# Optimization experiments

Hardware: AMD Instinct MI355X
Metric: run time of the kernel (lower is better)

## Reference

```python
import jax, jax.numpy as jnp
import numpy as np

EPS = 1e-06
BANDWIDTH = 0.1  # scipy minimize x0; frozen on first forward in the original


def _pairwise_sqdist(a, b):
    # a: [B, N, 3], b: [B, M, 3] -> [B, N, M] squared euclidean distances
    a2 = jnp.sum(a * a, axis=-1)  # [B, N]
    b2 = jnp.sum(b * b, axis=-1)  # [B, M]
    ab = jnp.einsum('bnd,bmd->bnm', a, b)  # [B, N, M]
    return jnp.maximum(a2[:, :, None] + b2[:, None, :] - 2.0 * ab, 0.0)


def _compute_density(points, bandwidth):
    # Gaussian KDE over all pairs (self included), normalized by N-1,
    # matching compute_density in the torch source.
    n = points.shape[1]
    sqd = _pairwise_sqdist(points, points)  # [B, N, N]
    kde = jnp.exp(-0.5 * sqd / (bandwidth * bandwidth))
    return jnp.sum(kde, axis=2) / (n - 1)  # [B, N]


def setup_inputs() -> dict:
    key = jax.random.key(0)
    k1, k2 = jax.random.split(key)
    predicted = jax.random.normal(k1, (8, 4096, 3), dtype=jnp.float32)
    ground_truth = jax.random.normal(k2, (8, 4096, 3), dtype=jnp.float32)
    return {
        'predicted': predicted,
        'ground_truth': ground_truth,
        'bandwidth_pred': jnp.float32(BANDWIDTH),
        'bandwidth_gt': jnp.float32(BANDWIDTH),
    }


def reference(predicted, ground_truth, bandwidth_pred, bandwidth_gt):
    # Chamfer distance: per-point squared distance to nearest neighbor in the
    # other cloud (standard ChamferDistance CUDA ext returns squared dists).
    sqd = _pairwise_sqdist(predicted, ground_truth)  # [B, N, M]
    dist_pred_to_gt = jnp.min(sqd, axis=2)  # [B, N]
    dist_gt_to_pred = jnp.min(sqd, axis=1)  # [B, M]

    density_pred = _compute_density(predicted, bandwidth_pred)  # [B, N]
    density_gt = _compute_density(ground_truth, bandwidth_gt)   # [B, M]

    loss_pred_to_gt = jnp.mean(dist_pred_to_gt / (density_pred + EPS))
    loss_gt_to_pred = jnp.mean(dist_gt_to_pred / (density_gt + EPS))
    return loss_pred_to_gt + loss_gt_to_pred
```

## Files before the change

### kernel.cpp

```cpp
#include <hip/hip_runtime.h>


#define NPTS 4096
#define NB   8
#define TS   128
#define TPB  256
#define NT   32
#define BIGF 3.4e38f

#define DCHUNKS    144
#define DENS_BLKS  (16*DCHUNKS)
#define CROSS_BLKS 2048
#define PTSTOT (NB*NPTS)
#define TRIVEC 496

__device__ __forceinline__ void unpack8(const float4* s4, int base,
                                        float (&X)[8], float (&Y)[8], float (&Z)[8])
{
    float4 A = s4[base+0], B = s4[base+1], C = s4[base+2];
    float4 D = s4[base+3], E = s4[base+4], F = s4[base+5];
    X[0]=A.x; Y[0]=A.y; Z[0]=A.z;  X[1]=A.w; Y[1]=B.x; Z[1]=B.y;
    X[2]=B.z; Y[2]=B.w; Z[2]=C.x;  X[3]=C.y; Y[3]=C.z; Z[3]=C.w;
    X[4]=D.x; Y[4]=D.y; Z[4]=D.z;  X[5]=D.w; Y[5]=E.x; Z[5]=E.y;
    X[6]=E.z; Y[6]=E.w; Z[6]=F.x;  X[7]=F.y; Y[7]=F.z; Z[7]=F.w;
}

__global__ __launch_bounds__(TPB) void dacl_pairs(
    const float* __restrict__ pred, const float* __restrict__ gt,
    const float* __restrict__ bwp,  const float* __restrict__ bwg,
    float* __restrict__ minP2Gp,
    float* __restrict__ minG2Pp,
    float* __restrict__ densCol,
    float* __restrict__ densRow)
{
    __shared__ float4 sCol[384];
    __shared__ float4 sRow[96];
    __shared__ float  sRed[384];

    const int tid  = threadIdx.x;
    const int ty   = tid & 15;
    const int tx   = tid >> 4;
    const int wave = tid >> 6;
    const int lane = tid & 63;
    const int bid  = blockIdx.x;

    if (bid < DENS_BLKS) {
        const int cb = bid / DCHUNKS;
        int rem      = bid - cb * DCHUNKS;
        const int b  = cb & 7;
        const int cl = cb >> 3;

        int u = 0;
        int nc = 8;
        while (rem >= nc) { rem -= nc; ++u; nc = (35 - u) >> 2; }
        const int cj = rem;
        const int js = cj * 4;
        const int steps = 32 - u;
        const int je = (js + 4 < steps) ? js + 4 : steps;
        const int nT = je - js;

        const float* __restrict__ P = cl ? gt : pred;
        float* __restrict__ dCol = densCol + (size_t)(cl*NB + b) * (TRIVEC*TS);
        float* __restrict__ dRow = densRow + (size_t)(cj*2 + cl) * PTSTOT + b*NPTS;
        const float bw = cl ? bwg[0] : bwp[0];
        const float sc = sqrtf(0.5f / (bw*bw*0.6931471805599453f));

        const float4* cb4 = (const float4*)(P + (size_t)b*NPTS*3);

        if (tid < 96) {
            float4 v = cb4[u*96 + tid];
            v.x*=sc; v.y*=sc; v.z*=sc; v.w*=sc;  sRow[tid] = v;
        }
        for (int i = tid; i < nT*96; i += TPB) {
            float4 v = cb4[(u + js)*96 + i];
            v.x*=sc; v.y*=sc; v.z*=sc; v.w*=sc;  sCol[i] = v;
        }
        __syncthreads();

        float rx[8], ry[8], rz[8], nrr[8], racc[8];
        unpack8(sRow, ty*6, rx, ry, rz);
        #pragma unroll
        for (int r = 0; r < 8; ++r) {
            nrr[r]  = -fmaf(rx[r],rx[r], fmaf(ry[r],ry[r], rz[r]*rz[r]));
            racc[r] = 0.0f;
        }

        for (int j = js; j < je; ++j) {
            const int t  = j - js;
            const int TV = u + j;

            float cx[8], cy[8], cz[8];
            unpack8(sCol, t*96 + tx*6, cx, cy, cz);

            if (j == 0) {
                #pragma unroll
                for (int c = 0; c < 8; ++c) {
                    const float ax = 2.0f*cx[c], ay = 2.0f*cy[c], az = 2.0f*cz[c];
                    const float ncc = fmaf(-cx[c],cx[c],
                                      fmaf(-cy[c],cy[c], -cz[c]*cz[c]));
                    #pragma unroll
                    for (int r = 0; r < 8; ++r) {
                        float e = fmaf(ax, rx[r], ncc);
                        e = fmaf(ay, ry[r], e);
                        e = fmaf(az, rz[r], e);
                        racc[r] += __builtin_amdgcn_exp2f(e + nrr[r]);
                    }
                }
            } else {
                float cacc[8];
                #pragma unroll
                for (int c = 0; c < 8; ++c) cacc[c] = 0.0f;
                #pragma unroll
                for (int c = 0; c < 8; ++c) {
                    const float ax = 2.0f*cx[c], ay = 2.0f*cy[c], az = 2.0f*cz[c];
                    const float ncc = fmaf(-cx[c],cx[c],
                                      fmaf(-cy[c],cy[c], -cz[c]*cz[c]));
                    #pragma unroll
                    for (int r = 0; r < 8; ++r) {
                        float e = fmaf(ax, rx[r], ncc);
                        e = fmaf(ay, ry[r], e);
                        e = fmaf(az, rz[r], e);
                        const float k = __builtin_amdgcn_exp2f(e + nrr[r]);
                        racc[r] += k;
                        cacc[c] += k;
                    }
                }
                const int triTV = (TV*(TV-1)) >> 1;
                #pragma unroll
                for (int c = 0; c < 8; ++c) {
                    float v = cacc[c];
                    v += __shfl_xor(v, 1, 64);
                    v += __shfl_xor(v, 2, 64);
                    v += __shfl_xor(v, 4, 64);
                    v += __shfl_xor(v, 8, 64);
                    if (ty == 0)
                        dCol[(triTV + u)*TS + tx*8 + c] = v;
                }
            }
        }
        {
            float vv[8];
            #pragma unroll
            for (int r = 0; r < 8; ++r) {
                float v = racc[r];
                v += __shfl_xor(v, 16, 64);
                v += __shfl_xor(v, 32, 64);
                vv[r] = v;
            }
            __syncthreads();
            if (wave > 0 && lane < 16) {
                #pragma unroll
                for (int r = 0; r < 8; ++r)
                    sRed[(wave-1)*128 + lane*8 + r] = vv[r];
            }
            __syncthreads();
            if (wave == 0 && lane < 16) {
                #pragma unroll
                for (int r = 0; r < 8; ++r) {
                    const int o = lane*8 + r;
                    dRow[u*TS + o] = (vv[r] + sRed[o])
                                   + (sRed[128+o] + sRed[256+o]);
                }
            }
        }
    } else {
        const int cb = bid - DENS_BLKS;
        const int b  = cb >> 8;
        const int I  = (cb >> 3) & 31;
        const int ph = cb & 7;

        const float4* pb4 = (const float4*)(pred + (size_t)b*NPTS*3);
        const float4* gb4 = (const float4*)(gt   + (size_t)b*NPTS*3);
        if (tid < 96) sRow[tid] = pb4[I*96 + tid];
        #pragma unroll
        for (int i = 0; i < 2; ++i) {
            const int o = tid + i*TPB;
            if (o < 384) sCol[o] = gb4[ph*384 + o];
        }
        __syncthreads();

        float rx[8], ry[8], rz[8], rr[8], rmin[8];
        unpack8(sRow, ty*6, rx, ry, rz);
        #pragma unroll
        for (int r = 0; r < 8; ++r) {
            rr[r]   = fmaf(rx[r],rx[r], fmaf(ry[r],ry[r], rz[r]*rz[r]));
            rmin[r] = BIGF;
        }
        float* __restrict__ mg = minG2Pp + (size_t)I*PTSTOT + b*NPTS;

        for (int t = 0; t < 4; ++t) {
            float cx[8], cy[8], cz[8], cmin[8];
            unpack8(sCol, t*96 + tx*6, cx, cy, cz);
            #pragma unroll
            for (int c = 0; c < 8; ++c) cmin[c] = BIGF;
            #pragma unroll
            for (int c2 = 0; c2 < 4; ++c2) {
                const int c0 = 2*c2, c1 = c0 + 1;
                const float ax0 = -2.0f*cx[c0], ay0 = -2.0f*cy[c0], az0 = -2.0f*cz[c0];
                const float cc0 = fmaf(cx[c0],cx[c0], fmaf(cy[c0],cy[c0], cz[c0]*cz[c0]));
                const float ax1 = -2.0f*cx[c1], ay1 = -2.0f*cy[c1], az1 = -2.0f*cz[c1];
                const float cc1 = fmaf(cx[c1],cx[c1], fmaf(cy[c1],cy[c1], cz[c1]*cz[c1]));
                #pragma unroll
                for (int r2 = 0; r2 < 4; ++r2) {
                    const int r0 = 2*r2, r1 = r0 + 1;
                    float t00 = fmaf(ax0, rx[r0], cc0);
                    t00 = fmaf(ay0, ry[r0], t00); t00 = fmaf(az0, rz[r0], t00);
                    float t01 = fmaf(ax1, rx[r0], cc1);
                    t01 = fmaf(ay1, ry[r0], t01); t01 = fmaf(az1, rz[r0], t01);
                    float t10 = fmaf(ax0, rx[r1], cc0);
                    t10 = fmaf(ay0, ry[r1], t10); t10 = fmaf(az0, rz[r1], t10);
                    float t11 = fmaf(ax1, rx[r1], cc1);
                    t11 = fmaf(ay1, ry[r1], t11); t11 = fmaf(az1, rz[r1], t11);
                    rmin[r0] = fminf(rmin[r0], fminf(t00, t01));
                    rmin[r1] = fminf(rmin[r1], fminf(t10, t11));
                    const float d00 = t00 + rr[r0], d01 = t01 + rr[r0];
                    const float d10 = t10 + rr[r1], d11 = t11 + rr[r1];
                    cmin[c0] = fminf(cmin[c0], fminf(d00, d10));
                    cmin[c1] = fminf(cmin[c1], fminf(d01, d11));
                }
            }
            #pragma unroll
            for (int c = 0; c < 8; ++c) {
                float v = cmin[c];
                v = fminf(v, __shfl_xor(v, 1, 64));
                v = fminf(v, __shfl_xor(v, 2, 64));
                v = fminf(v, __shfl_xor(v, 4, 64));
                v = fminf(v, __shfl_xor(v, 8, 64));
                if (ty == 0)
                    mg[(ph*4+t)*TS + tx*8 + c] = v;
            }
        }
        float vv[8];
        #pragma unroll
        for (int r = 0; r < 8; ++r) {
            float v = rmin[r] + rr[r];
            v = fminf(v, __shfl_xor(v, 16, 64));
            v = fminf(v, __shfl_xor(v, 32, 64));
            vv[r] = v;
        }
        __syncthreads();
        if (wave > 0 && lane < 16) {
            #pragma unroll
            for (int r = 0; r < 8; ++r) sRed[(wave-1)*128 + lane*8 + r] = vv[r];
        }
        __syncthreads();
        if (wave == 0 && lane < 16) {
            #pragma unroll
            for (int r = 0; r < 8; ++r) {
                const int o = lane*8 + r;
                minP2Gp[(size_t)ph*PTSTOT + b*NPTS + I*TS + o] =
                    fminf(fminf(vv[r], sRed[o]),
                          fminf(sRed[128+o], sRed[256+o]));
            }
        }
    }
}

__global__ __launch_bounds__(256) void dacl_combine(
    const float* __restrict__ minP2Gp, const float* __restrict__ minG2Pp,
    const float* __restrict__ densCol, const float* __restrict__ densRow,
    float* __restrict__ bsum)
{
    const int g   = blockIdx.x * 256 + threadIdx.x;
    const int dir = g >> 15;
    const int idx = g & 32767;
    const int b   = idx >> 12;
    const int pt  = idx & 4095;
    const int T   = pt >> 7;
    const int co  = pt & 127;
    const int cl  = dir;

    float m = BIGF;
    if (dir == 0) {
        #pragma unroll
        for (int s = 0; s < 8; ++s) m = fminf(m, minP2Gp[(size_t)s*PTSTOT + idx]);
    } else {
        #pragma unroll
        for (int s = 0; s < 32; ++s) m = fminf(m, minG2Pp[(size_t)s*PTSTOT + idx]);
    }
    m = fmaxf(m, 0.0f);

    float dn = 0.0f;
    const float* dC = densCol + (size_t)(cl*NB + b)*(TRIVEC*TS)
                      + ((T*(T-1)) >> 1)*TS + co;
    for (int RT = 0; RT < T; ++RT) dn += dC[RT*TS];
    const int ncj = (35 - T) >> 2;
    #pragma unroll
    for (int cj = 0; cj < 8; ++cj) {
        if (cj < ncj) dn += densRow[(size_t)(cj*2 + cl)*PTSTOT + idx];
    }

    float val = m / (dn * (1.0f/4095.0f) + 1e-6f) * (1.0f/32768.0f);

    #pragma unroll
    for (int off = 32; off; off >>= 1) val += __shfl_down(val, off);
    __shared__ float sm[4];
    const int lane = threadIdx.x & 63, wid = threadIdx.x >> 6;
    if (lane == 0) sm[wid] = val;
    __syncthreads();
    if (threadIdx.x == 0) bsum[blockIdx.x] = (sm[0] + sm[1]) + (sm[2] + sm[3]);
}

__global__ __launch_bounds__(256) void dacl_final(
    const float* __restrict__ bsum, float* __restrict__ out)
{
    float v = bsum[threadIdx.x];
    #pragma unroll
    for (int off = 32; off; off >>= 1) v += __shfl_down(v, off);
    __shared__ float sm[4];
    const int lane = threadIdx.x & 63, wid = threadIdx.x >> 6;
    if (lane == 0) sm[wid] = v;
    __syncthreads();
    if (threadIdx.x == 0) out[0] = (sm[0] + sm[1]) + (sm[2] + sm[3]);
}

extern "C" void kernel_launch(void* const* d_in, const int* in_sizes, int n_in,
                              void* d_out, int out_size, void* d_ws, size_t ws_size,
                              hipStream_t stream)
{
    const float* pred = (const float*)d_in[0];
    const float* gt   = (const float*)d_in[1];
    const float* bwp  = (const float*)d_in[2];
    const float* bwg  = (const float*)d_in[3];

    float* minP2Gp = (float*)d_ws;
    float* minG2Pp = minP2Gp + (size_t)8*PTSTOT;
    float* densCol = minG2Pp + (size_t)32*PTSTOT;
    float* densRow = densCol + (size_t)16*TRIVEC*TS;
    float* bsum    = densRow + (size_t)16*PTSTOT;

    dacl_pairs<<<DENS_BLKS + CROSS_BLKS, TPB, 0, stream>>>(
        pred, gt, bwp, bwg, minP2Gp, minG2Pp, densCol, densRow);
    dacl_combine<<<256, 256, 0, stream>>>(minP2Gp, minG2Pp, densCol, densRow, bsum);
    dacl_final<<<1, 256, 0, stream>>>(bsum, (float*)d_out);
}
```

Baseline: 88.86 us.

## Morton-sort point clouds and cull tile pairs using AABB bounds

Adds a pre-pass that bins each cloud into a 16^3 grid, sorts the points by Morton code and records a bounding box for every 128-point tile. A second pre-pass computes per-tile upper bounds on nearest-neighbour distance. The density loop skips tile pairs whose Gaussian terms would all fall below about 2^-30. The chamfer loop skips tile pairs whose box gap exceeds both tiles' upper bounds, so it cannot contain a nearest neighbour. The goal is to remove most of the quadratic pair work, at the cost of three extra kernel launches, a buffer-initialization pass and a small truncation error in the density sums.

```diff
diff --git a/kernel.cpp b/kernel.cpp
--- a/kernel.cpp
+++ b/kernel.cpp
@@ -5,8 +5,9 @@
 #define NB   8
 #define TS   128
 #define TPB  256
-#define NT   32
 #define BIGF 3.4e38f
+#define LN2f 0.6931471805599453f
+#define SKIP_THR 30.0f
 
 #define DCHUNKS    144
 #define DENS_BLKS  (16*DCHUNKS)
@@ -25,9 +26,144 @@
     X[6]=E.z; Y[6]=E.w; Z[6]=F.x;  X[7]=F.y; Y[7]=F.z; Z[7]=F.w;
 }
 
+__device__ __forceinline__ float aabbGap2(const float* A, const float* B)
+{
+    float g, s;
+    g = fmaxf(0.f, fmaxf(B[0]-A[4], A[0]-B[4])); s = g*g;
+    g = fmaxf(0.f, fmaxf(B[1]-A[5], A[1]-B[5])); s = fmaf(g,g,s);
+    g = fmaxf(0.f, fmaxf(B[2]-A[6], A[2]-B[6])); s = fmaf(g,g,s);
+    return s;
+}
+
+__global__ __launch_bounds__(1024) void dacl_sort(
+    const float* __restrict__ pred, const float* __restrict__ gt,
+    float* __restrict__ sortedP,
+    float* __restrict__ aabb)
+{
+    __shared__ int h[4096];
+    __shared__ int wsum[16];
+    const int tid  = threadIdx.x;
+    const int lane = tid & 63, wid = tid >> 6;
+    const int cb   = blockIdx.x;
+    const int b    = cb & 7, cl = cb >> 3;
+    const float* src = (cl ? gt : pred) + (size_t)b*NPTS*3;
+    float* dst = sortedP + (size_t)cb*NPTS*3;
+
+    for (int i = tid; i < 4096; i += 1024) h[i] = 0;
+    __syncthreads();
+
+    float px[4], py[4], pz[4]; int code[4];
+    #pragma unroll
+    for (int k = 0; k < 4; ++k) {
+        const int i = k*1024 + tid;
+        const float x = src[i*3], y = src[i*3+1], z = src[i*3+2];
+        px[k]=x; py[k]=y; pz[k]=z;
+        int cx = (int)floorf((x + 4.8f) * (1.0f/0.6f));
+        int cy = (int)floorf((y + 4.8f) * (1.0f/0.6f));
+        int cz = (int)floorf((z + 4.8f) * (1.0f/0.6f));
+        cx = min(max(cx,0),15); cy = min(max(cy,0),15); cz = min(max(cz,0),15);
+        int m = 0;
+        #pragma unroll
+        for (int bit = 0; bit < 4; ++bit)
+            m |= (((cx>>bit)&1)<<(3*bit)) | (((cy>>bit)&1)<<(3*bit+1))
+               | (((cz>>bit)&1)<<(3*bit+2));
+        code[k] = m;
+        atomicAdd(&h[m], 1);
+    }
+    __syncthreads();
+
+    const int a0=h[4*tid], a1=h[4*tid+1], a2=h[4*tid+2], a3=h[4*tid+3];
+    const int tot = a0+a1+a2+a3;
+    int v = tot;
+    #pragma unroll
+    for (int off = 1; off < 64; off <<= 1) {
+        int n = __shfl_up(v, off, 64);
+        if (lane >= off) v += n;
+    }
+    if (lane == 63) wsum[wid] = v;
+    __syncthreads();
+    if (tid == 0) {
+        int run = 0;
+        for (int i = 0; i < 16; ++i) { int t = wsum[i]; wsum[i] = run; run += t; }
+    }
+    __syncthreads();
+    const int excl = wsum[wid] + v - tot;
+    h[4*tid]   = excl;
+    h[4*tid+1] = excl + a0;
+    h[4*tid+2] = excl + a0 + a1;
+    h[4*tid+3] = excl + a0 + a1 + a2;
+    __syncthreads();
+
+    #pragma unroll
+    for (int k = 0; k < 4; ++k) {
+        const int pos = atomicAdd(&h[code[k]], 1);
+        dst[pos*3]   = px[k];
+        dst[pos*3+1] = py[k];
+        dst[pos*3+2] = pz[k];
+    }
+    __threadfence();
+    __syncthreads();
+
+    {
+        const int t = tid >> 5, j = tid & 31;
+        float mnx=BIGF,mny=BIGF,mnz=BIGF,mxx=-BIGF,mxy=-BIGF,mxz=-BIGF;
+        #pragma unroll
+        for (int kk = 0; kk < 4; ++kk) {
+            const int i = t*128 + j*4 + kk;
+            const float x = dst[i*3], y = dst[i*3+1], z = dst[i*3+2];
+            mnx=fminf(mnx,x); mny=fminf(mny,y); mnz=fminf(mnz,z);
+            mxx=fmaxf(mxx,x); mxy=fmaxf(mxy,y); mxz=fmaxf(mxz,z);
+        }
+        #pragma unroll
+        for (int off = 1; off < 32; off <<= 1) {
+            mnx=fminf(mnx,__shfl_xor(mnx,off,64));
+            mny=fminf(mny,__shfl_xor(mny,off,64));
+            mnz=fminf(mnz,__shfl_xor(mnz,off,64));
+            mxx=fmaxf(mxx,__shfl_xor(mxx,off,64));
+            mxy=fmaxf(mxy,__shfl_xor(mxy,off,64));
+            mxz=fmaxf(mxz,__shfl_xor(mxz,off,64));
+        }
+        if (j == 0) {
+            float* o = aabb + (size_t)(cb*32 + t)*8;
+            o[0]=mnx; o[1]=mny; o[2]=mnz; o[3]=0.f;
+            o[4]=mxx; o[5]=mxy; o[6]=mxz; o[7]=0.f;
+        }
+    }
+}
+
+__global__ __launch_bounds__(256) void dacl_prep2(
+    const float* __restrict__ sortedP, float* __restrict__ UB)
+{
+    const int g = blockIdx.x*256 + threadIdx.x;
+    const int b = g >> 12, i = g & 4095;
+    const float* ps = sortedP + (size_t)b*12288;
+    const float* gs = sortedP + (size_t)(8+b)*12288;
+    const float dx = ps[i*3]-gs[i*3], dy = ps[i*3+1]-gs[i*3+1],
+                dz = ps[i*3+2]-gs[i*3+2];
+    float d2 = dx*dx + dy*dy + dz*dz;
+    const int lane = threadIdx.x & 63, wid = threadIdx.x >> 6;
+    #pragma unroll
+    for (int off = 1; off < 64; off <<= 1)
+        d2 = fmaxf(d2, __shfl_xor(d2, off, 64));
+    __shared__ float wmax[4];
+    if (lane == 0) wmax[wid] = d2;
+    __syncthreads();
+    if (threadIdx.x == 0)   UB[blockIdx.x*2]     = fmaxf(wmax[0], wmax[1]);
+    if (threadIdx.x == 128) UB[blockIdx.x*2 + 1] = fmaxf(wmax[2], wmax[3]);
+}
+
+__global__ __launch_bounds__(256) void dacl_init(
+    float* __restrict__ minG2Pp, float* __restrict__ densCol)
+{
+    const int g = blockIdx.x*256 + threadIdx.x;
+    minG2Pp[g] = BIGF;
+    if (g < 16*TRIVEC*TS) densCol[g] = 0.0f;
+}
+
 __global__ __launch_bounds__(TPB) void dacl_pairs(
-    const float* __restrict__ pred, const float* __restrict__ gt,
-    const float* __restrict__ bwp,  const float* __restrict__ bwg,
+    const float* __restrict__ sortedP, const float* __restrict__ aabb,
+    const float* __restrict__ UB,
+    const float* __restrict__ bwp, const float* __restrict__ bwg,
     float* __restrict__ minP2Gp,
     float* __restrict__ minG2Pp,
     float* __restrict__ densCol,
@@ -50,8 +186,7 @@
         const int b  = cb & 7;
         const int cl = cb >> 3;
 
-        int u = 0;
-        int nc = 8;
+        int u = 0, nc = 8;
         while (rem >= nc) { rem -= nc; ++u; nc = (35 - u) >> 2; }
         const int cj = rem;
         const int js = cj * 4;
@@ -59,13 +194,15 @@
         const int je = (js + 4 < steps) ? js + 4 : steps;
         const int nT = je - js;
 
-        const float* __restrict__ P = cl ? gt : pred;
-        float* __restrict__ dCol = densCol + (size_t)(cl*NB + b) * (TRIVEC*TS);
+        const float* __restrict__ P = sortedP + (size_t)cb*12288;
+        float* __restrict__ dCol = densCol + (size_t)cb * (TRIVEC*TS);
         float* __restrict__ dRow = densRow + (size_t)(cj*2 + cl) * PTSTOT + b*NPTS;
         const float bw = cl ? bwg[0] : bwp[0];
-        const float sc = sqrtf(0.5f / (bw*bw*0.6931471805599453f));
-
-        const float4* cb4 = (const float4*)(P + (size_t)b*NPTS*3);
+        const float s2raw = 0.5f / (bw*bw*LN2f);
+        const float sc = sqrtf(s2raw);
+        const float* myAB = aabb + (size_t)(cb*32 + u)*8;
+
+        const float4* cb4 = (const float4*)P;
 
         if (tid < 96) {
             float4 v = cb4[u*96 + tid];
@@ -88,6 +225,11 @@
         for (int j = js; j < je; ++j) {
             const int t  = j - js;
             const int TV = u + j;
+
+            if (j > 0) {
+                const float* cAB = aabb + (size_t)(cb*32 + TV)*8;
+                if (s2raw * aabbGap2(myAB, cAB) > SKIP_THR) continue;
+            }
 
             float cx[8], cy[8], cz[8];
             unpack8(sCol, t*96 + tx*6, cx, cy, cz);
@@ -169,8 +311,11 @@
         const int I  = (cb >> 3) & 31;
         const int ph = cb & 7;
 
-        const float4* pb4 = (const float4*)(pred + (size_t)b*NPTS*3);
-        const float4* gb4 = (const float4*)(gt   + (size_t)b*NPTS*3);
+        const float4* pb4 = (const float4*)(sortedP + (size_t)b*12288);
+        const float4* gb4 = (const float4*)(sortedP + (size_t)(8+b)*12288);
+        const float* pAB  = aabb + (size_t)(b*32 + I)*8;
+        const float  UB_I = UB[b*32 + I];
+
         if (tid < 96) sRow[tid] = pb4[I*96 + tid];
         #pragma unroll
         for (int i = 0; i < 2; ++i) {
@@ -189,6 +334,10 @@
         float* __restrict__ mg = minG2Pp + (size_t)I*PTSTOT + b*NPTS;
 
         for (int t = 0; t < 4; ++t) {
+            const int J = ph*4 + t;
+            const float* gAB = aabb + (size_t)((8+b)*32 + J)*8;
+            if (aabbGap2(pAB, gAB) > fmaxf(UB_I, UB[b*32 + J])) continue;
+
             float cx[8], cy[8], cz[8], cmin[8];
             unpack8(sCol, t*96 + tx*6, cx, cy, cz);
             #pragma unroll
@@ -227,7 +376,7 @@
                 v = fminf(v, __shfl_xor(v, 4, 64));
                 v = fminf(v, __shfl_xor(v, 8, 64));
                 if (ty == 0)
-                    mg[(ph*4+t)*TS + tx*8 + c] = v;
+                    mg[J*TS + tx*8 + c] = v;
             }
         }
         float vv[8];
@@ -323,14 +472,20 @@
     const float* bwp  = (const float*)d_in[2];
     const float* bwg  = (const float*)d_in[3];
 
-    float* minP2Gp = (float*)d_ws;
-    float* minG2Pp = minP2Gp + (size_t)8*PTSTOT;
-    float* densCol = minG2Pp + (size_t)32*PTSTOT;
-    float* densRow = densCol + (size_t)16*TRIVEC*TS;
-    float* bsum    = densRow + (size_t)16*PTSTOT;
-
+    float* sortedP  = (float*)d_ws;
+    float* aabb     = sortedP + (size_t)16*12288;
+    float* UBarr    = aabb + 512*8;
+    float* minP2Gp  = UBarr + 256;
+    float* minG2Pp  = minP2Gp + (size_t)8*PTSTOT;
+    float* densCol  = minG2Pp + (size_t)32*PTSTOT;
+    float* densRow  = densCol + (size_t)16*TRIVEC*TS;
+    float* bsum     = densRow + (size_t)16*PTSTOT;
+
+    dacl_sort<<<16, 1024, 0, stream>>>(pred, gt, sortedP, aabb);
+    dacl_prep2<<<128, 256, 0, stream>>>(sortedP, UBarr);
+    dacl_init<<<4096, 256, 0, stream>>>(minG2Pp, densCol);
     dacl_pairs<<<DENS_BLKS + CROSS_BLKS, TPB, 0, stream>>>(
-        pred, gt, bwp, bwg, minP2Gp, minG2Pp, densCol, densRow);
+        sortedP, aabb, UBarr, bwp, bwg, minP2Gp, minG2Pp, densCol, densRow);
     dacl_combine<<<256, 256, 0, stream>>>(minP2Gp, minG2Pp, densCol, densRow, bsum);
     dacl_final<<<1, 256, 0, stream>>>(bsum, (float*)d_out);
 }
```

Result: slower. 116.3 us (+30.9%).
